# Optimization experiments

Hardware: AMD Instinct MI355X
Metric: run time of the kernel (lower is better)

## Reference

```python
import jax, jax.numpy as jnp
import numpy as np

H, W, NF, K, MD, ND, NDM, MLP_H = 128, 128, 8, 9, 16, 8, 8, 64
NPIX = H * W
RADIUS = int((K ** 0.5 - 1) // 2)


def _compute_neighbors_adjusted(height, width, radius):
    # Faithful port of LocalResiduals._compute_neighbors_adjusted (setup-time only).
    Kn = (2 * radius + 1) ** 2
    base = np.stack(np.meshgrid(np.arange(-radius, radius + 1),
                                np.arange(-radius, radius + 1), indexing='ij'),
                    axis=-1).reshape(-1, 2)
    neighbors = np.empty((height * width, Kn), dtype=np.int64)
    for i in range(height):
        for j in range(width):
            off = base.copy()
            ni = i + off[:, 0]
            nj = j + off[:, 1]
            valid = (ni >= 0) & (ni < height) & (nj >= 0) & (nj < width)
            valid_inds = list(ni[valid] * width + nj[valid])
            expansion = 1
            while len(valid_inds) < Kn:
                r_ext = radius + expansion
                ext = np.stack(np.meshgrid(np.arange(-r_ext, r_ext + 1),
                                           np.arange(-r_ext, r_ext + 1), indexing='ij'),
                               axis=-1).reshape(-1, 2)
                seen = set(map(tuple, off.tolist()))
                ext_new = np.array([t for t in map(tuple, ext.tolist()) if t not in seen],
                                   dtype=np.int64)
                off = np.concatenate([off, ext_new], axis=0)
                ni_e = i + ext_new[:, 0]
                nj_e = j + ext_new[:, 1]
                valid_e = (ni_e >= 0) & (ni_e < height) & (nj_e >= 0) & (nj_e < width)
                valid_inds += list(ni_e[valid_e] * width + nj_e[valid_e])
                expansion += 1
            neighbors[i * width + j] = np.array(valid_inds[:Kn], dtype=np.int64)
    return neighbors


def setup_inputs() -> dict:
    key = jax.random.key(0)
    ks = jax.random.split(key, 8)
    B = 16
    y_in = jax.random.normal(ks[0], (B, NF, H, W), dtype=jnp.float32)
    noise = jax.random.normal(ks[1], (B, ND, NPIX), dtype=jnp.float32)
    noise2 = jax.random.normal(ks[2], (B, NPIX, NDM), dtype=jnp.float32)
    n_in = NF + ND
    # xavier-uniform-like init for weight_map
    bound = float(np.sqrt(6.0 / (MD + n_in)))
    weight_map = jax.random.uniform(ks[3], (NPIX, K, MD, n_in), dtype=jnp.float32,
                                    minval=-bound, maxval=bound)
    d0 = MD + NDM
    w1 = jax.random.normal(ks[4], (MLP_H, d0), dtype=jnp.float32) / np.sqrt(d0)
    b1 = jnp.zeros((MLP_H,), dtype=jnp.float32)
    w2 = jax.random.normal(ks[5], (NF, MLP_H), dtype=jnp.float32) / np.sqrt(MLP_H)
    b2 = jnp.zeros((NF,), dtype=jnp.float32)
    neighbor_idx = jnp.asarray(_compute_neighbors_adjusted(H, W, RADIUS))  # (NPIX, K)
    return {"y_in": y_in, "noise": noise, "noise2": noise2,
            "weight_map": weight_map, "w1": w1, "b1": b1, "w2": w2, "b2": b2,
            "neighbor_idx": neighbor_idx}


def reference(y_in, noise, noise2, weight_map, w1, b1, w2, b2, neighbor_idx):
    B = y_in.shape[0]
    y_flat = y_in.reshape(B, NF, NPIX)
    y_with_noise = jnp.concatenate([y_flat, noise], axis=1)        # (B, NF+ND, NPIX)
    feats = jnp.transpose(y_with_noise, (0, 2, 1))                  # (B, NPIX, NF+ND)
    gather_y = feats[:, neighbor_idx, :]                            # (B, NPIX, K, NF+ND)
    # per-pixel distinct weight contraction
    intermediate = jnp.einsum('bpkn,pkmn->bpm', gather_y, weight_map)  # (B, NPIX, MD)
    mlp_in = jnp.concatenate([intermediate, noise2], axis=-1)      # (B, NPIX, MD+NDM)
    h = jax.nn.relu(jnp.einsum('bpd,hd->bph', mlp_in, w1) + b1)
    out = jnp.einsum('bph,fh->bpf', h, w2) + b2                    # (B, NPIX, NF)
    out = jnp.transpose(out, (0, 2, 1)).reshape(B, NF, H, W)
    return out
```

## Files before the change

### kernel.cpp

```cpp
#include <hip/hip_runtime.h>

#define NPIX 16384

typedef _Float16 f16;
typedef __attribute__((ext_vector_type(8))) _Float16 half8;
typedef __attribute__((ext_vector_type(8))) unsigned short ushort8;
typedef __attribute__((ext_vector_type(4))) float f32x4;
typedef __attribute__((ext_vector_type(2))) float f32x2;

__device__ inline half8 cvt8_nt(const float* __restrict__ p) {
  f32x4 a = __builtin_nontemporal_load((const f32x4*)p);
  f32x4 b = __builtin_nontemporal_load((const f32x4*)p + 1);
  half8 r;
  r[0] = (f16)a.x; r[1] = (f16)a.y; r[2] = (f16)a.z; r[3] = (f16)a.w;
  r[4] = (f16)b.x; r[5] = (f16)b.y; r[6] = (f16)b.z; r[7] = (f16)b.w;
  return r;
}
__device__ inline half8 cvt8(const float* __restrict__ p) {
  f32x4 a = *(const f32x4*)p;
  f32x4 b = *(const f32x4*)(p + 4);
  half8 r;
  r[0] = (f16)a.x; r[1] = (f16)a.y; r[2] = (f16)a.z; r[3] = (f16)a.w;
  r[4] = (f16)b.x; r[5] = (f16)b.y; r[6] = (f16)b.z; r[7] = (f16)b.w;
  return r;
}

__global__ __launch_bounds__(256) void pack_feats(
    const float* __restrict__ y,
    const float* __restrict__ nz,
    const float* __restrict__ nz2,
    f16* __restrict__ outf,
    f16* __restrict__ n2p)
{
  __shared__ f16 tile[64][258];
  const int p0 = blockIdx.x << 6;
  const int t = threadIdx.x;
  const int lane16 = t & 15;
  const int pl0 = t >> 4;
  #pragma unroll
  for (int g = 0; g < 16; ++g) {
    const int plane = g * 16 + pl0;
    const int b = plane >> 4, n = plane & 15;
    const float* src = (n < 8) ? (y + (b * 8 + n) * NPIX)
                               : (nz + (b * 8 + (n - 8)) * NPIX);
    f32x4 v = __builtin_nontemporal_load((const f32x4*)(src + p0 + lane16 * 4));
    tile[lane16 * 4 + 0][plane] = (f16)v.x;
    tile[lane16 * 4 + 1][plane] = (f16)v.y;
    tile[lane16 * 4 + 2][plane] = (f16)v.z;
    tile[lane16 * 4 + 3][plane] = (f16)v.w;
  }
  #pragma unroll
  for (int it = 0; it < 4; ++it) {
    const int pair = it * 256 + t;
    const int b = pair >> 6;
    const int pl = pair & 63;
    half8 v = cvt8_nt(nz2 + (size_t)(b * NPIX + p0 + pl) * 8);
    *(half8*)(n2p + (p0 + pl) * 128 + b * 8) = v;
  }
  __syncthreads();
  #pragma unroll
  for (int it = 0; it < 8; ++it) {
    const int idx = it * 256 + t;
    const int px = idx >> 5;
    const int c = idx & 31;
    ushort8 v = *(const ushort8*)&tile[px][c * 8];
    *(ushort8*)(outf + (p0 + px) * 256 + c * 8) = v;
  }
}

__global__ __launch_bounds__(256, 4) void lr_fused(
    const f16*  __restrict__ feats,
    const f16*  __restrict__ n2p,
    const float* __restrict__ wmap,
    const int*  __restrict__ nidx,
    const float* __restrict__ w1,
    const float* __restrict__ b1,
    const float* __restrict__ w2,
    const float* __restrict__ b2,
    float* __restrict__ outp)
{
  __shared__ f16 tbuf[4][256];
  __shared__ f16 lds_h[4][16 * 72];
  __shared__ __align__(16) float stage[128][4];

  const int t = threadIdx.x;
  const int wv = t >> 6;
  const int l = t & 63;
  const int col = l & 15;
  const int q = l >> 4;

  const int bid = blockIdx.x;
  const int p0 = ((((bid & 7) << 9) + (bid >> 3)) << 2);
  const int p = p0 + wv;

  const int n0 = (q & 1) * 8;
  const int kh = q >> 1;

  const int ps = __builtin_amdgcn_readfirstlane(p);
  int nb[9];
  #pragma unroll
  for (int k = 0; k < 9; ++k)
    nb[k] = __builtin_amdgcn_readfirstlane(nidx[ps * 9 + k]);

  half8 af[5], bfr[5];
  #pragma unroll
  for (int c = 0; c < 4; ++c) {
    const int k = 2 * c + kh;
    af[c]  = *(const half8*)(feats + nb[k] * 256 + col * 16 + n0);
    bfr[c] = cvt8_nt(wmap + ((ps * 9 + k) * 16 + col) * 16 + n0);
  }
  af[4]  = (half8){0, 0, 0, 0, 0, 0, 0, 0};
  bfr[4] = (half8){0, 0, 0, 0, 0, 0, 0, 0};
  if (q < 2) {
    af[4]  = *(const half8*)(feats + nb[8] * 256 + col * 16 + n0);
    bfr[4] = cvt8_nt(wmap + ((ps * 9 + 8) * 16 + col) * 16 + n0);
  }
  f32x4 acc = {0.f, 0.f, 0.f, 0.f};
  #pragma unroll
  for (int c = 0; c < 5; ++c)
    acc = __builtin_amdgcn_mfma_f32_16x16x32_f16(af[c], bfr[c], acc, 0, 0, 0);

  f16* tb = tbuf[wv];
  #pragma unroll
  for (int r = 0; r < 4; ++r)
    tb[(q * 4 + r) * 16 + col] = (f16)acc[r];

  half8 w1f[4];
  float b1f[4];
  #pragma unroll
  for (int jc = 0; jc < 4; ++jc) {
    w1f[jc] = (half8){0, 0, 0, 0, 0, 0, 0, 0};
    if (q < 3) w1f[jc] = cvt8(w1 + (jc * 16 + col) * 24 + q * 8);
    b1f[jc] = b1[jc * 16 + col];
  }
  half8 w2f[2] = {{0, 0, 0, 0, 0, 0, 0, 0}, {0, 0, 0, 0, 0, 0, 0, 0}};
  float b2f = 0.f;
  if (col < 8) {
    w2f[0] = cvt8(w2 + col * 64 + q * 8);
    w2f[1] = cvt8(w2 + col * 64 + 32 + q * 8);
    b2f = b2[col];
  }
  half8 n2v = (half8){0, 0, 0, 0, 0, 0, 0, 0};
  if (q == 2) n2v = *(const half8*)(n2p + p * 128 + col * 8);

  const f32x4 zero4 = {0.f, 0.f, 0.f, 0.f};

  half8 amlp = n2v;
  if (q < 2) amlp = *(const half8*)(tb + col * 16 + q * 8);

  f16* lh = lds_h[wv];
  #pragma unroll
  for (int jc = 0; jc < 4; ++jc) {
    f32x4 h4 = __builtin_amdgcn_mfma_f32_16x16x32_f16(amlp, w1f[jc], zero4, 0, 0, 0);
    #pragma unroll
    for (int r = 0; r < 4; ++r) {
      float hv = fmaxf(h4[r] + b1f[jc], 0.f);
      lh[(q * 4 + r) * 72 + jc * 16 + col] = (f16)hv;
    }
  }

  f32x4 oacc = zero4;
  #pragma unroll
  for (int c2 = 0; c2 < 2; ++c2) {
    half8 a2 = *(const half8*)(lh + col * 72 + c2 * 32 + q * 8);
    oacc = __builtin_amdgcn_mfma_f32_16x16x32_f16(a2, w2f[c2], oacc, 0, 0, 0);
  }
  if (col < 8) {
    #pragma unroll
    for (int r = 0; r < 4; ++r) {
      const int row = q * 32 + r * 8 + col;
      stage[row][wv] = oacc[r] + b2f;
    }
  }

  __syncthreads();

  {
    const int row = t >> 1;
    const int h2 = (t & 1) * 2;
    f32x2 v = *(const f32x2*)&stage[row][h2];
    *(f32x2*)(outp + row * NPIX + p0 + h2) = v;
  }
}

extern "C" void kernel_launch(void* const* d_in, const int* in_sizes, int n_in,
                              void* d_out, int out_size, void* d_ws, size_t ws_size,
                              hipStream_t stream) {
  const float* y    = (const float*)d_in[0];
  const float* nz   = (const float*)d_in[1];
  const float* nz2  = (const float*)d_in[2];
  const float* wmap = (const float*)d_in[3];
  const float* w1   = (const float*)d_in[4];
  const float* b1   = (const float*)d_in[5];
  const float* w2   = (const float*)d_in[6];
  const float* b2   = (const float*)d_in[7];
  const int* nidx   = (const int*)d_in[8];
  float* outp = (float*)d_out;
  f16* feats = (f16*)d_ws;
  f16* n2p   = (f16*)((char*)d_ws + (size_t)NPIX * 256 * 2);

  hipLaunchKernelGGL(pack_feats, dim3(NPIX / 64), dim3(256), 0, stream,
                     y, nz, nz2, feats, n2p);
  hipLaunchKernelGGL(lr_fused, dim3(NPIX / 4), dim3(256), 0, stream,
                     feats, n2p, wmap, nidx, w1, b1, w2, b2, outp);
}
```

Before: 248.7 us.

## Process two pixels per wave in fused local-residual kernel

Each wave now handles two adjacent pixels instead of one, halving the grid size. Loads for both pixels' gathered features and per-pixel weights are issued up front and their MFMAs are interleaved, so more memory requests are in flight per wave. MLP weight loads are amortized across two pixels, and output stores widen to 16-byte vectors. Register pressure rises, so launch bounds drop to 3 blocks per SM, which may lower occupancy.

```diff
diff --git a/kernel.cpp b/kernel.cpp
--- a/kernel.cpp
+++ b/kernel.cpp
@@ -6,7 +6,6 @@
 typedef __attribute__((ext_vector_type(8))) _Float16 half8;
 typedef __attribute__((ext_vector_type(8))) unsigned short ushort8;
 typedef __attribute__((ext_vector_type(4))) float f32x4;
-typedef __attribute__((ext_vector_type(2))) float f32x2;
 
 __device__ inline half8 cvt8_nt(const float* __restrict__ p) {
   f32x4 a = __builtin_nontemporal_load((const f32x4*)p);
@@ -68,7 +67,7 @@
   }
 }
 
-__global__ __launch_bounds__(256, 4) void lr_fused(
+__global__ __launch_bounds__(256, 3) void lr_fused(
     const f16*  __restrict__ feats,
     const f16*  __restrict__ n2p,
     const float* __restrict__ wmap,
@@ -79,9 +78,9 @@
     const float* __restrict__ b2,
     float* __restrict__ outp)
 {
-  __shared__ f16 tbuf[4][256];
+  __shared__ f16 tbuf[4][2][256];
   __shared__ f16 lds_h[4][16 * 72];
-  __shared__ __align__(16) float stage[128][4];
+  __shared__ __align__(16) float stage[128][8];
 
   const int t = threadIdx.x;
   const int wv = t >> 6;
@@ -90,40 +89,58 @@
   const int q = l >> 4;
 
   const int bid = blockIdx.x;
-  const int p0 = ((((bid & 7) << 9) + (bid >> 3)) << 2);
-  const int p = p0 + wv;
+  const int p0 = (((bid & 7) << 8) + (bid >> 3)) << 3;
+  const int pw = p0 + wv * 2;
 
   const int n0 = (q & 1) * 8;
   const int kh = q >> 1;
 
-  const int ps = __builtin_amdgcn_readfirstlane(p);
-  int nb[9];
-  #pragma unroll
-  for (int k = 0; k < 9; ++k)
-    nb[k] = __builtin_amdgcn_readfirstlane(nidx[ps * 9 + k]);
-
-  half8 af[5], bfr[5];
+  const int ps = __builtin_amdgcn_readfirstlane(pw);
+  int nb0[9], nb1[9];
+  #pragma unroll
+  for (int k = 0; k < 9; ++k) {
+    nb0[k] = __builtin_amdgcn_readfirstlane(nidx[ps * 9 + k]);
+    nb1[k] = __builtin_amdgcn_readfirstlane(nidx[ps * 9 + 9 + k]);
+  }
+
+  half8 af0[5], bf0[5], af1[5], bf1[5];
   #pragma unroll
   for (int c = 0; c < 4; ++c) {
     const int k = 2 * c + kh;
-    af[c]  = *(const half8*)(feats + nb[k] * 256 + col * 16 + n0);
-    bfr[c] = cvt8_nt(wmap + ((ps * 9 + k) * 16 + col) * 16 + n0);
-  }
-  af[4]  = (half8){0, 0, 0, 0, 0, 0, 0, 0};
-  bfr[4] = (half8){0, 0, 0, 0, 0, 0, 0, 0};
+    af0[c] = *(const half8*)(feats + nb0[k] * 256 + col * 16 + n0);
+    bf0[c] = cvt8_nt(wmap + ((ps * 9 + k) * 16 + col) * 16 + n0);
+  }
+  #pragma unroll
+  for (int c = 0; c < 4; ++c) {
+    const int k = 2 * c + kh;
+    af1[c] = *(const half8*)(feats + nb1[k] * 256 + col * 16 + n0);
+    bf1[c] = cvt8_nt(wmap + (((ps + 1) * 9 + k) * 16 + col) * 16 + n0);
+  }
+  af0[4] = (half8){0, 0, 0, 0, 0, 0, 0, 0};
+  bf0[4] = (half8){0, 0, 0, 0, 0, 0, 0, 0};
+  af1[4] = (half8){0, 0, 0, 0, 0, 0, 0, 0};
+  bf1[4] = (half8){0, 0, 0, 0, 0, 0, 0, 0};
   if (q < 2) {
-    af[4]  = *(const half8*)(feats + nb[8] * 256 + col * 16 + n0);
-    bfr[4] = cvt8_nt(wmap + ((ps * 9 + 8) * 16 + col) * 16 + n0);
-  }
-  f32x4 acc = {0.f, 0.f, 0.f, 0.f};
-  #pragma unroll
-  for (int c = 0; c < 5; ++c)
-    acc = __builtin_amdgcn_mfma_f32_16x16x32_f16(af[c], bfr[c], acc, 0, 0, 0);
-
-  f16* tb = tbuf[wv];
-  #pragma unroll
-  for (int r = 0; r < 4; ++r)
-    tb[(q * 4 + r) * 16 + col] = (f16)acc[r];
+    af0[4] = *(const half8*)(feats + nb0[8] * 256 + col * 16 + n0);
+    bf0[4] = cvt8_nt(wmap + ((ps * 9 + 8) * 16 + col) * 16 + n0);
+    af1[4] = *(const half8*)(feats + nb1[8] * 256 + col * 16 + n0);
+    bf1[4] = cvt8_nt(wmap + (((ps + 1) * 9 + 8) * 16 + col) * 16 + n0);
+  }
+  f32x4 acc0 = {0.f, 0.f, 0.f, 0.f};
+  f32x4 acc1 = {0.f, 0.f, 0.f, 0.f};
+  #pragma unroll
+  for (int c = 0; c < 5; ++c) {
+    acc0 = __builtin_amdgcn_mfma_f32_16x16x32_f16(af0[c], bf0[c], acc0, 0, 0, 0);
+    acc1 = __builtin_amdgcn_mfma_f32_16x16x32_f16(af1[c], bf1[c], acc1, 0, 0, 0);
+  }
+
+  f16* tb0 = tbuf[wv][0];
+  f16* tb1 = tbuf[wv][1];
+  #pragma unroll
+  for (int r = 0; r < 4; ++r) {
+    tb0[(q * 4 + r) * 16 + col] = (f16)acc0[r];
+    tb1[(q * 4 + r) * 16 + col] = (f16)acc1[r];
+  }
 
   half8 w1f[4];
   float b1f[4];
@@ -140,36 +157,43 @@
     w2f[1] = cvt8(w2 + col * 64 + 32 + q * 8);
     b2f = b2[col];
   }
-  half8 n2v = (half8){0, 0, 0, 0, 0, 0, 0, 0};
-  if (q == 2) n2v = *(const half8*)(n2p + p * 128 + col * 8);
+  half8 n2v[2] = {{0, 0, 0, 0, 0, 0, 0, 0}, {0, 0, 0, 0, 0, 0, 0, 0}};
+  if (q == 2) {
+    n2v[0] = *(const half8*)(n2p + pw * 128 + col * 8);
+    n2v[1] = *(const half8*)(n2p + (pw + 1) * 128 + col * 8);
+  }
 
   const f32x4 zero4 = {0.f, 0.f, 0.f, 0.f};
-
-  half8 amlp = n2v;
-  if (q < 2) amlp = *(const half8*)(tb + col * 16 + q * 8);
-
   f16* lh = lds_h[wv];
-  #pragma unroll
-  for (int jc = 0; jc < 4; ++jc) {
-    f32x4 h4 = __builtin_amdgcn_mfma_f32_16x16x32_f16(amlp, w1f[jc], zero4, 0, 0, 0);
+
+  #pragma unroll
+  for (int px = 0; px < 2; ++px) {
+    half8 amlp = n2v[px];
+    if (q < 2) amlp = *(const half8*)(tbuf[wv][px] + col * 16 + q * 8);
+
     #pragma unroll
-    for (int r = 0; r < 4; ++r) {
-      float hv = fmaxf(h4[r] + b1f[jc], 0.f);
-      lh[(q * 4 + r) * 72 + jc * 16 + col] = (f16)hv;
+    for (int jc = 0; jc < 4; ++jc) {
+      f32x4 h4 = __builtin_amdgcn_mfma_f32_16x16x32_f16(amlp, w1f[jc], zero4, 0, 0, 0);
+      #pragma unroll
+      for (int r = 0; r < 4; ++r) {
+        float hv = fmaxf(h4[r] + b1f[jc], 0.f);
+        lh[(q * 4 + r) * 72 + jc * 16 + col] = (f16)hv;
+      }
     }
-  }
-
-  f32x4 oacc = zero4;
-  #pragma unroll
-  for (int c2 = 0; c2 < 2; ++c2) {
-    half8 a2 = *(const half8*)(lh + col * 72 + c2 * 32 + q * 8);
-    oacc = __builtin_amdgcn_mfma_f32_16x16x32_f16(a2, w2f[c2], oacc, 0, 0, 0);
-  }
-  if (col < 8) {
+
+    f32x4 oacc = zero4;
     #pragma unroll
-    for (int r = 0; r < 4; ++r) {
-      const int row = q * 32 + r * 8 + col;
-      stage[row][wv] = oacc[r] + b2f;
+    for (int c2 = 0; c2 < 2; ++c2) {
+      half8 a2 = *(const half8*)(lh + col * 72 + c2 * 32 + q * 8);
+      oacc = __builtin_amdgcn_mfma_f32_16x16x32_f16(a2, w2f[c2], oacc, 0, 0, 0);
+    }
+    if (col < 8) {
+      const int pxl = wv * 2 + px;
+      #pragma unroll
+      for (int r = 0; r < 4; ++r) {
+        const int row = q * 32 + r * 8 + col;
+        stage[row][pxl] = oacc[r] + b2f;
+      }
     }
   }
 
@@ -177,9 +201,9 @@
 
   {
     const int row = t >> 1;
-    const int h2 = (t & 1) * 2;
-    f32x2 v = *(const f32x2*)&stage[row][h2];
-    *(f32x2*)(outp + row * NPIX + p0 + h2) = v;
+    const int c4 = (t & 1) * 4;
+    f32x4 v = *(const f32x4*)&stage[row][c4];
+    *(f32x4*)(outp + row * NPIX + p0 + c4) = v;
   }
 }
 
@@ -201,6 +225,6 @@
 
   hipLaunchKernelGGL(pack_feats, dim3(NPIX / 64), dim3(256), 0, stream,
                      y, nz, nz2, feats, n2p);
-  hipLaunchKernelGGL(lr_fused, dim3(NPIX / 4), dim3(256), 0, stream,
+  hipLaunchKernelGGL(lr_fused, dim3(NPIX / 8), dim3(256), 0, stream,
                      feats, n2p, wmap, nidx, w1, b1, w2, b2, outp);
 }
```

After: 257.2 us. 1.03x slower.
